# Performance work log

Hardware: AMD Instinct MI355X
Metric: run time of the kernel (lower is better)

## Reference

```python
import jax, jax.numpy as jnp
import numpy as np

N_NODES = 40000


def _sage_conv(x, edge_index, W_l, W_r, b, num_nodes):
    # PyG SAGEConv (mean aggr): out = lin_l(mean_{j in N(i)} x_j) + lin_r(x_i)
    src, dst = edge_index[0], edge_index[1]
    msgs = x[src]                                            # [E, F] gather
    sums = jax.ops.segment_sum(msgs, dst, num_segments=num_nodes)
    counts = jax.ops.segment_sum(jnp.ones((src.shape[0],), x.dtype), dst,
                                 num_segments=num_nodes)
    mean = sums / jnp.maximum(counts, 1.0)[:, None]          # [N, F]
    return mean @ W_l + b + x @ W_r


def setup_inputs() -> dict:
    key = jax.random.key(0)
    ks = jax.random.split(key, 8)
    in_c, hid_c, out_c = 128, 256, 128
    x = jax.random.normal(ks[0], (N_NODES, in_c), dtype=jnp.float32)
    edge_index = jax.random.randint(ks[1], (2, 640000), 0, N_NODES, dtype=jnp.int64)
    s1 = 1.0 / np.sqrt(in_c)
    s2 = 1.0 / np.sqrt(hid_c)
    return {
        "x": x,
        "edge_index": edge_index,
        "W1_l": jax.random.uniform(ks[2], (in_c, hid_c), jnp.float32, -s1, s1),
        "W1_r": jax.random.uniform(ks[3], (in_c, hid_c), jnp.float32, -s1, s1),
        "b1": jnp.zeros((hid_c,), jnp.float32),
        "W2_l": jax.random.uniform(ks[4], (hid_c, out_c), jnp.float32, -s2, s2),
        "W2_r": jax.random.uniform(ks[5], (hid_c, out_c), jnp.float32, -s2, s2),
        "b2": jnp.zeros((out_c,), jnp.float32),
    }


def reference(x, edge_index, W1_l, W1_r, b1, W2_l, W2_r, b2):
    h = _sage_conv(x, edge_index, W1_l, W1_r, b1, N_NODES)
    h = jax.nn.relu(h)
    out = _sage_conv(h, edge_index, W2_l, W2_r, b2, N_NODES)
    return out
```

## Files before the change

kernel.cpp:

```cpp
#include <hip/hip_runtime.h>


constexpr int F1  = 128;
constexpr int HID = 256;

typedef __attribute__((ext_vector_type(8))) short   short8;
typedef __attribute__((ext_vector_type(8))) ushort  us8;
typedef __attribute__((ext_vector_type(4))) ushort  us4;
typedef __attribute__((ext_vector_type(4))) float   f32x4;

__device__ __forceinline__ ushort f2bf(float f) {
  unsigned u = __float_as_uint(f);
  return (ushort)((u + 0x7fffu + ((u >> 16) & 1u)) >> 16);
}
__device__ __forceinline__ float bf2f_lo(unsigned v) { return __uint_as_float(v << 16); }
__device__ __forceinline__ float bf2f_hi(unsigned v) { return __uint_as_float(v & 0xffff0000u); }

#define GLOAD_LDS16(gsrc, ldst)                                                  \
  __builtin_amdgcn_global_load_lds(                                              \
      (const __attribute__((address_space(1))) void*)(gsrc),                     \
      (__attribute__((address_space(3))) void*)(ldst), 16, 0, 0)

__global__ void deg_kernel(const int* __restrict__ dst, int* __restrict__ deg, int E) {
  int i = (blockIdx.x * blockDim.x + threadIdx.x) * 2;
  if (i + 1 < E) {
    int2 d = *(const int2*)(dst + i);
    atomicAdd(deg + d.x, 1);
    atomicAdd(deg + d.y, 1);
  } else if (i < E) {
    atomicAdd(deg + dst[i], 1);
  }
}

__global__ __launch_bounds__(256) void scan_part(const int* __restrict__ deg,
                                                 int* __restrict__ bsum, int N) {
  __shared__ int sm[256];
  int t = threadIdx.x;
  int base = blockIdx.x * 1024 + t * 4;
  int s = 0;
  if (base + 3 < N) {
    int4 v = *(const int4*)(deg + base);
    s = v.x + v.y + v.z + v.w;
  } else {
    for (int q = 0; q < 4; ++q) if (base + q < N) s += deg[base + q];
  }
  sm[t] = s;
  __syncthreads();
  for (int d = 128; d; d >>= 1) {
    if (t < d) sm[t] += sm[t + d];
    __syncthreads();
  }
  if (t == 0) bsum[blockIdx.x] = sm[0];
}

__global__ void scan_bsum(const int* __restrict__ bsum, int* __restrict__ boff,
                          int* __restrict__ off, int N, int nb) {
  int t = threadIdx.x;
  int v = (t < nb) ? bsum[t] : 0;
  int inc = v;
  for (int d = 1; d < 64; d <<= 1) {
    int u = __shfl_up(inc, d);
    if (t >= d) inc += u;
  }
  if (t < nb) boff[t] = inc - v;
  if (t == 63) off[N] = inc;
}

__global__ __launch_bounds__(256) void scan_emit(const int* __restrict__ deg,
                                                 const int* __restrict__ boff,
                                                 int* __restrict__ off,
                                                 int* __restrict__ cursor, int N) {
  __shared__ int sm[256];
  int t = threadIdx.x;
  int base = blockIdx.x * 1024 + t * 4;
  int d0 = 0, d1 = 0, d2 = 0, d3 = 0;
  if (base + 3 < N) {
    int4 v = *(const int4*)(deg + base);
    d0 = v.x; d1 = v.y; d2 = v.z; d3 = v.w;
  } else {
    if (base + 0 < N) d0 = deg[base + 0];
    if (base + 1 < N) d1 = deg[base + 1];
    if (base + 2 < N) d2 = deg[base + 2];
    if (base + 3 < N) d3 = deg[base + 3];
  }
  int s = d0 + d1 + d2 + d3;
  sm[t] = s;
  __syncthreads();
  for (int d = 1; d < 256; d <<= 1) {
    int u = (t >= d) ? sm[t - d] : 0;
    __syncthreads();
    sm[t] += u;
    __syncthreads();
  }
  int o0 = (t ? sm[t - 1] : 0) + boff[blockIdx.x];
  int o1 = o0 + d0, o2 = o1 + d1, o3 = o2 + d2;
  if (base + 3 < N) {
    int4 o = make_int4(o0, o1, o2, o3);
    *(int4*)(off + base) = o;
    *(int4*)(cursor + base) = o;
  } else {
    if (base + 0 < N) { off[base + 0] = o0; cursor[base + 0] = o0; }
    if (base + 1 < N) { off[base + 1] = o1; cursor[base + 1] = o1; }
    if (base + 2 < N) { off[base + 2] = o2; cursor[base + 2] = o2; }
    if (base + 3 < N) { off[base + 3] = o3; cursor[base + 3] = o3; }
  }
}

__global__ void fill_kernel(const int* __restrict__ src, const int* __restrict__ dst,
                            int* __restrict__ cursor, int* __restrict__ csr, int E) {
  int i = blockIdx.x * blockDim.x + threadIdx.x;
  if (i < E) {
    int p = atomicAdd(cursor + dst[i], 1);
    csr[p] = src[i];
  }
}

__global__ void xcvt_kernel(const float* __restrict__ x, ushort* __restrict__ Ab,
                            int* __restrict__ deg, int N) {
  int i = blockIdx.x * blockDim.x + threadIdx.x;
  if (i < N) deg[i] = 0;
  if (i >= N * 16) return;
  int row = i >> 4, c = (i & 15) * 8;
  const float* p = x + (size_t)row * F1 + c;
  us8 o;
#pragma unroll
  for (int j = 0; j < 8; ++j) o[j] = f2bf(p[j]);
  *(us8*)(Ab + (size_t)row * HID + 128 + c) = o;
}

__global__ void wcvt_kernel(const float* __restrict__ W1l, const float* __restrict__ W1r,
                            const float* __restrict__ W2l, const float* __restrict__ W2r,
                            ushort* __restrict__ B1t, ushort* __restrict__ B2t) {
  int i = blockIdx.x * blockDim.x + threadIdx.x;
  if (i >= 16384) return;
  int which = i >> 13;
  int j = i & 8191;
  int n = j >> 5;
  int kb = (j & 31) * 8;
  us8 o;
  if (which == 0) {
#pragma unroll
    for (int q = 0; q < 8; ++q) {
      int k = kb + q;
      float v = (k < 128) ? W1l[k * HID + n] : W1r[(k - 128) * HID + n];
      o[q] = f2bf(v);
    }
    *(us8*)(B1t + n * HID + kb) = o;
  } else {
#pragma unroll
    for (int q = 0; q < 8; ++q) {
      int k = kb + q;
      float v = (n < 128) ? W2l[k * F1 + n] : W2r[k * F1 + (n - 128)];
      o[q] = f2bf(v);
    }
    *(us8*)(B2t + n * HID + kb) = o;
  }
}


__device__ __forceinline__ void acc8(float* acc, const uint4 v) {
  acc[0] += bf2f_lo(v.x); acc[1] += bf2f_hi(v.x);
  acc[2] += bf2f_lo(v.y); acc[3] += bf2f_hi(v.y);
  acc[4] += bf2f_lo(v.z); acc[5] += bf2f_hi(v.z);
  acc[6] += bf2f_lo(v.w); acc[7] += bf2f_hi(v.w);
}

__global__ __launch_bounds__(256) void agg1_kernel(const int* __restrict__ off,
                                                   const int* __restrict__ csr,
                                                   ushort* __restrict__ Ab, int N) {
  const int t = threadIdx.x;
  const int w = t >> 6, l = t & 63;
  const int g = l >> 4, sub = l & 15;
  const int node = blockIdx.x * 16 + w * 4 + g;
  if (node >= N) return;
  const int s = off[node], e = off[node + 1];
  float acc[8] = {0.f, 0.f, 0.f, 0.f, 0.f, 0.f, 0.f, 0.f};
  const int cb = sub * 8;
  const int4* csr4 = (const int4*)csr;
  int k0 = s & ~7;
  int4 c0 = csr4[(k0 >> 2) + 0];
  int4 c1 = csr4[(k0 >> 2) + 1];
#define ROW1(j) (*(const uint4*)(Ab + (size_t)(j) * HID + 128 + cb))
  for (int k = k0; k < e; k += 8) {
    int4 n0 = csr4[(k >> 2) + 2];
    int4 n1 = csr4[(k >> 2) + 3];
    if (k + 0 >= s && k + 0 < e) acc8(acc, ROW1(c0.x));
    if (k + 1 >= s && k + 1 < e) acc8(acc, ROW1(c0.y));
    if (k + 2 >= s && k + 2 < e) acc8(acc, ROW1(c0.z));
    if (k + 3 >= s && k + 3 < e) acc8(acc, ROW1(c0.w));
    if (k + 4 >= s && k + 4 < e) acc8(acc, ROW1(c1.x));
    if (k + 5 >= s && k + 5 < e) acc8(acc, ROW1(c1.y));
    if (k + 6 >= s && k + 6 < e) acc8(acc, ROW1(c1.z));
    if (k + 7 < e)               acc8(acc, ROW1(c1.w));
    c0 = n0; c1 = n1;
  }
#undef ROW1
  int d = e - s; if (d < 1) d = 1;
  float inv = 1.0f / (float)d;
  us8 o;
#pragma unroll
  for (int q = 0; q < 8; ++q) o[q] = f2bf(acc[q] * inv);
  *(us8*)(Ab + (size_t)node * HID + cb) = o;
}

__global__ __launch_bounds__(256) void agg2_kernel(const ushort* __restrict__ y2,
                                                   const int* __restrict__ off,
                                                   const int* __restrict__ csr,
                                                   float* __restrict__ out, int N) {
  const int t = threadIdx.x;
  const int w = t >> 6, l = t & 63;
  const int g = l >> 4, sub = l & 15;
  const int node = blockIdx.x * 16 + w * 4 + g;
  if (node >= N) return;
  const int s = off[node], e = off[node + 1];
  float acc[8] = {0.f, 0.f, 0.f, 0.f, 0.f, 0.f, 0.f, 0.f};
  const int cb = sub * 8;
  const int4* csr4 = (const int4*)csr;
  int k0 = s & ~7;
  int4 c0 = csr4[(k0 >> 2) + 0];
  int4 c1 = csr4[(k0 >> 2) + 1];
#define ROW2(j) (*(const uint4*)(y2 + (size_t)(j) * F1 + cb))
  for (int k = k0; k < e; k += 8) {
    int4 n0 = csr4[(k >> 2) + 2];
    int4 n1 = csr4[(k >> 2) + 3];
    if (k + 0 >= s && k + 0 < e) acc8(acc, ROW2(c0.x));
    if (k + 1 >= s && k + 1 < e) acc8(acc, ROW2(c0.y));
    if (k + 2 >= s && k + 2 < e) acc8(acc, ROW2(c0.z));
    if (k + 3 >= s && k + 3 < e) acc8(acc, ROW2(c0.w));
    if (k + 4 >= s && k + 4 < e) acc8(acc, ROW2(c1.x));
    if (k + 5 >= s && k + 5 < e) acc8(acc, ROW2(c1.y));
    if (k + 6 >= s && k + 6 < e) acc8(acc, ROW2(c1.z));
    if (k + 7 < e)               acc8(acc, ROW2(c1.w));
    c0 = n0; c1 = n1;
  }
#undef ROW2
  int d = e - s; if (d < 1) d = 1;
  float inv = 1.0f / (float)d;
  float* po = out + (size_t)node * F1 + cb;
  float4 z0 = *(const float4*)(po);
  float4 z1 = *(const float4*)(po + 4);
  z0.x += acc[0] * inv; z0.y += acc[1] * inv; z0.z += acc[2] * inv; z0.w += acc[3] * inv;
  z1.x += acc[4] * inv; z1.y += acc[5] * inv; z1.z += acc[6] * inv; z1.w += acc[7] * inv;
  *(float4*)(po)     = z0;
  *(float4*)(po + 4) = z1;
}

template <int MODE>
__global__ __launch_bounds__(256) void gemm_kernel(
    const ushort* __restrict__ A, const ushort* __restrict__ Bt,
    const float* __restrict__ bias, ushort* __restrict__ Cb,
    float* __restrict__ Cf, int M) {
  constexpr int K = 256, BK = 64;
  __shared__ __align__(16) ushort As[128 * 64];
  __shared__ __align__(16) ushort Bs[128 * 64];
  const int t = threadIdx.x;
  const int l = t & 63;
  const int w = t >> 6;
  const int m0 = blockIdx.x * 128;
  const int n0 = blockIdx.y * 128;
  const int wr = (w & 1) * 64;
  const int wc = (w >> 1) * 64;

  const int sk = (((l & 7) ^ (l >> 3)) << 3);
  const int rsub = l >> 3;

  f32x4 acc[4][4];
  const f32x4 zero = {0.f, 0.f, 0.f, 0.f};
#pragma unroll
  for (int mi = 0; mi < 4; ++mi)
#pragma unroll
    for (int ni = 0; ni < 4; ++ni) acc[mi][ni] = zero;

  for (int k0 = 0; k0 < K; k0 += BK) {
    if (k0) __syncthreads();
#pragma unroll
    for (int q = 0; q < 4; ++q) {
      int r = w * 32 + q * 8 + rsub;
      int ar = m0 + r; if (ar >= M) ar = M - 1;
      GLOAD_LDS16(A + (size_t)ar * K + k0 + sk, &As[w * 2048 + q * 512]);
      GLOAD_LDS16(Bt + (size_t)(n0 + r) * K + k0 + sk, &Bs[w * 2048 + q * 512]);
    }
    __syncthreads();
#pragma unroll
    for (int ks = 0; ks < 2; ++ks) {
      short8 af[4], bfr[4];
      const int kin = ks * 64 + ((l >> 4) << 4);
#pragma unroll
      for (int i = 0; i < 4; ++i) {
        int rA = wr + i * 16 + (l & 15);
        af[i] = *(const short8*)((const char*)As + rA * 128 + (kin ^ ((rA & 7) << 4)));
        int rB = wc + i * 16 + (l & 15);
        bfr[i] = *(const short8*)((const char*)Bs + rB * 128 + (kin ^ ((rB & 7) << 4)));
      }
#pragma unroll
      for (int mi = 0; mi < 4; ++mi)
#pragma unroll
        for (int ni = 0; ni < 4; ++ni)
          acc[mi][ni] = __builtin_amdgcn_mfma_f32_16x16x32_bf16(bfr[ni], af[mi], acc[mi][ni], 0, 0, 0);
    }
  }

#pragma unroll
  for (int ni = 0; ni < 4; ++ni) {
    const int cn = wc + ni * 16 + ((l >> 4) << 2);
    float4 bb = make_float4(0.f, 0.f, 0.f, 0.f);
    if (MODE == 1) bb = *(const float4*)(bias + n0 + cn);
    if (MODE == 2 && n0 != 0) bb = *(const float4*)(bias + cn);
#pragma unroll
    for (int mi = 0; mi < 4; ++mi) {
      int row = m0 + wr + mi * 16 + (l & 15);
      if (row >= M) continue;
      f32x4 v = acc[mi][ni];
      if (MODE == 1) {
        us4 o;
        o[0] = f2bf(fmaxf(v[0] + bb.x, 0.f));
        o[1] = f2bf(fmaxf(v[1] + bb.y, 0.f));
        o[2] = f2bf(fmaxf(v[2] + bb.z, 0.f));
        o[3] = f2bf(fmaxf(v[3] + bb.w, 0.f));
        *(us4*)(Cb + (size_t)row * HID + n0 + cn) = o;
      } else if (n0 == 0) {
        us4 o;
        o[0] = f2bf(v[0]); o[1] = f2bf(v[1]); o[2] = f2bf(v[2]); o[3] = f2bf(v[3]);
        *(us4*)(Cb + (size_t)row * F1 + cn) = o;
      } else {
        float4 o;
        o.x = v[0] + bb.x; o.y = v[1] + bb.y; o.z = v[2] + bb.z; o.w = v[3] + bb.w;
        *(float4*)(Cf + (size_t)row * F1 + cn) = o;
      }
    }
  }
}

extern "C" void kernel_launch(void* const* d_in, const int* in_sizes, int n_in,
                              void* d_out, int out_size, void* d_ws, size_t ws_size,
                              hipStream_t stream) {
  const float* x   = (const float*)d_in[0];
  const int* edge  = (const int*)d_in[1];
  const float* W1l = (const float*)d_in[2];
  const float* W1r = (const float*)d_in[3];
  const float* b1  = (const float*)d_in[4];
  const float* W2l = (const float*)d_in[5];
  const float* W2r = (const float*)d_in[6];
  const float* b2  = (const float*)d_in[7];
  float* out = (float*)d_out;

  const int N = in_sizes[0] / F1;
  const int E = in_sizes[1] / 2;
  const int* src = edge;
  const int* dst = edge + E;

  uintptr_t p = (uintptr_t)d_ws;
  auto alloc = [&](size_t bytes) -> void* {
    void* r = (void*)p;
    p += (bytes + 255) & ~(size_t)255;
    return r;
  };
  int* deg      = (int*)alloc((size_t)N * 4);
  int* off      = (int*)alloc((size_t)(N + 1) * 4);
  int* cursor   = (int*)alloc((size_t)N * 4);
  int* csr      = (int*)alloc((size_t)(E + 16) * 4);
  int* bsum     = (int*)alloc(64 * 4);
  int* boff     = (int*)alloc(64 * 4);
  ushort* Abf   = (ushort*)alloc((size_t)N * HID * 2);
  ushort* h     = (ushort*)alloc((size_t)N * HID * 2);
  ushort* y2    = (ushort*)alloc((size_t)N * F1 * 2);
  ushort* B1t   = (ushort*)alloc((size_t)HID * HID * 2);
  ushort* B2t   = (ushort*)alloc((size_t)HID * HID * 2);
  (void)ws_size; (void)n_in; (void)out_size;

  wcvt_kernel<<<64, 256, 0, stream>>>(W1l, W1r, W2l, W2r, B1t, B2t);
  xcvt_kernel<<<(N * 16 + 255) / 256, 256, 0, stream>>>(x, Abf, deg, N);
  deg_kernel<<<(E / 2 + 255) / 256, 256, 0, stream>>>(dst, deg, E);

  const int nb = (N + 1023) / 1024;
  scan_part<<<nb, 256, 0, stream>>>(deg, bsum, N);
  scan_bsum<<<1, 64, 0, stream>>>(bsum, boff, off, N, nb);
  scan_emit<<<nb, 256, 0, stream>>>(deg, boff, off, cursor, N);

  fill_kernel<<<(E + 255) / 256, 256, 0, stream>>>(src, dst, cursor, csr, E);
  agg1_kernel<<<(N + 15) / 16, 256, 0, stream>>>(off, csr, Abf, N);

  dim3 gg((N + 127) / 128, 2);
  gemm_kernel<1><<<gg, 256, 0, stream>>>(Abf, B1t, b1, h, nullptr, N);
  gemm_kernel<2><<<gg, 256, 0, stream>>>(h, B2t, b2, y2, out, N);

  agg2_kernel<<<(N + 15) / 16, 256, 0, stream>>>(y2, off, csr, out, N);
}
```

Baseline: 239.0 us.

## Fuse both GEMMs into one kernel keeping hidden activations in LDS

Merges the two GEMM launches into one mlp_kernel that computes the 64-row hidden tile, applies bias and ReLU, stores it swizzled in LDS, then runs the second GEMM from LDS. This removes the global write and read of the N×256 bf16 hidden tensor and one launch. It also merges the weight and feature conversion kernels into one and folds the block-sum scan into scan_emit. The cost is a large LDS footprint (about 72 KB per block), which lowers occupancy, and B1/B2 are reloaded by every 64-row block.

```diff
diff --git a/kernel.cpp b/kernel.cpp
--- a/kernel.cpp
+++ b/kernel.cpp
@@ -20,6 +20,48 @@
   __builtin_amdgcn_global_load_lds(                                              \
       (const __attribute__((address_space(1))) void*)(gsrc),                     \
       (__attribute__((address_space(3))) void*)(ldst), 16, 0, 0)
+
+__global__ void prep_kernel(const float* __restrict__ x, ushort* __restrict__ Ab,
+                            int* __restrict__ deg,
+                            const float* __restrict__ W1l, const float* __restrict__ W1r,
+                            const float* __restrict__ W2l, const float* __restrict__ W2r,
+                            ushort* __restrict__ B1t, ushort* __restrict__ B2t, int N) {
+  int i = blockIdx.x * blockDim.x + threadIdx.x;
+  if (i < N) deg[i] = 0;
+  if (i < N * 16) {
+    int row = i >> 4, c = (i & 15) * 8;
+    const float* p = x + (size_t)row * F1 + c;
+    us8 o;
+#pragma unroll
+    for (int j = 0; j < 8; ++j) o[j] = f2bf(p[j]);
+    *(us8*)(Ab + (size_t)row * HID + 128 + c) = o;
+    return;
+  }
+  int j = i - N * 16;
+  if (j >= 16384) return;
+  int which = j >> 13;
+  int jj = j & 8191;
+  int n = jj >> 5;
+  int kb = (jj & 31) * 8;
+  us8 o;
+  if (which == 0) {
+#pragma unroll
+    for (int q = 0; q < 8; ++q) {
+      int k = kb + q;
+      float v = (k < 128) ? W1l[k * HID + n] : W1r[(k - 128) * HID + n];
+      o[q] = f2bf(v);
+    }
+    *(us8*)(B1t + n * HID + kb) = o;
+  } else {
+#pragma unroll
+    for (int q = 0; q < 8; ++q) {
+      int k = kb + q;
+      float v = (n < 128) ? W2l[k * F1 + n] : W2r[k * F1 + (n - 128)];
+      o[q] = f2bf(v);
+    }
+    *(us8*)(B2t + n * HID + kb) = o;
+  }
+}
 
 __global__ void deg_kernel(const int* __restrict__ dst, int* __restrict__ deg, int E) {
   int i = (blockIdx.x * blockDim.x + threadIdx.x) * 2;
@@ -53,25 +95,23 @@
   if (t == 0) bsum[blockIdx.x] = sm[0];
 }
 
-__global__ void scan_bsum(const int* __restrict__ bsum, int* __restrict__ boff,
-                          int* __restrict__ off, int N, int nb) {
+__global__ __launch_bounds__(256) void scan_emit(const int* __restrict__ deg,
+                                                 const int* __restrict__ bsum,
+                                                 int* __restrict__ off,
+                                                 int* __restrict__ cursor, int N, int nb) {
+  __shared__ int sm[256];
+  __shared__ int sboff;
   int t = threadIdx.x;
-  int v = (t < nb) ? bsum[t] : 0;
-  int inc = v;
-  for (int d = 1; d < 64; d <<= 1) {
-    int u = __shfl_up(inc, d);
-    if (t >= d) inc += u;
-  }
-  if (t < nb) boff[t] = inc - v;
-  if (t == 63) off[N] = inc;
-}
-
-__global__ __launch_bounds__(256) void scan_emit(const int* __restrict__ deg,
-                                                 const int* __restrict__ boff,
-                                                 int* __restrict__ off,
-                                                 int* __restrict__ cursor, int N) {
-  __shared__ int sm[256];
-  int t = threadIdx.x;
+  if (t < 64) {
+    int v = (t < nb) ? bsum[t] : 0;
+    int inc = v;
+    for (int d = 1; d < 64; d <<= 1) {
+      int u = __shfl_up(inc, d);
+      if (t >= d) inc += u;
+    }
+    if (t == (int)blockIdx.x) sboff = inc - v;
+    if ((int)blockIdx.x == (int)gridDim.x - 1 && t == 63) off[N] = inc;
+  }
   int base = blockIdx.x * 1024 + t * 4;
   int d0 = 0, d1 = 0, d2 = 0, d3 = 0;
   if (base + 3 < N) {
@@ -92,7 +132,7 @@
     sm[t] += u;
     __syncthreads();
   }
-  int o0 = (t ? sm[t - 1] : 0) + boff[blockIdx.x];
+  int o0 = (t ? sm[t - 1] : 0) + sboff;
   int o1 = o0 + d0, o2 = o1 + d1, o3 = o2 + d2;
   if (base + 3 < N) {
     int4 o = make_int4(o0, o1, o2, o3);
@@ -114,49 +154,6 @@
     csr[p] = src[i];
   }
 }
-
-__global__ void xcvt_kernel(const float* __restrict__ x, ushort* __restrict__ Ab,
-                            int* __restrict__ deg, int N) {
-  int i = blockIdx.x * blockDim.x + threadIdx.x;
-  if (i < N) deg[i] = 0;
-  if (i >= N * 16) return;
-  int row = i >> 4, c = (i & 15) * 8;
-  const float* p = x + (size_t)row * F1 + c;
-  us8 o;
-#pragma unroll
-  for (int j = 0; j < 8; ++j) o[j] = f2bf(p[j]);
-  *(us8*)(Ab + (size_t)row * HID + 128 + c) = o;
-}
-
-__global__ void wcvt_kernel(const float* __restrict__ W1l, const float* __restrict__ W1r,
-                            const float* __restrict__ W2l, const float* __restrict__ W2r,
-                            ushort* __restrict__ B1t, ushort* __restrict__ B2t) {
-  int i = blockIdx.x * blockDim.x + threadIdx.x;
-  if (i >= 16384) return;
-  int which = i >> 13;
-  int j = i & 8191;
-  int n = j >> 5;
-  int kb = (j & 31) * 8;
-  us8 o;
-  if (which == 0) {
-#pragma unroll
-    for (int q = 0; q < 8; ++q) {
-      int k = kb + q;
-      float v = (k < 128) ? W1l[k * HID + n] : W1r[(k - 128) * HID + n];
-      o[q] = f2bf(v);
-    }
-    *(us8*)(B1t + n * HID + kb) = o;
-  } else {
-#pragma unroll
-    for (int q = 0; q < 8; ++q) {
-      int k = kb + q;
-      float v = (n < 128) ? W2l[k * F1 + n] : W2r[k * F1 + (n - 128)];
-      o[q] = f2bf(v);
-    }
-    *(us8*)(B2t + n * HID + kb) = o;
-  }
-}
-
 
 __device__ __forceinline__ void acc8(float* acc, const uint4 v) {
   acc[0] += bf2f_lo(v.x); acc[1] += bf2f_hi(v.x);
@@ -245,22 +242,22 @@
   *(float4*)(po + 4) = z1;
 }
 
-template <int MODE>
-__global__ __launch_bounds__(256) void gemm_kernel(
-    const ushort* __restrict__ A, const ushort* __restrict__ Bt,
-    const float* __restrict__ bias, ushort* __restrict__ Cb,
-    float* __restrict__ Cf, int M) {
+__global__ __launch_bounds__(256) void mlp_kernel(
+    const ushort* __restrict__ A, const ushort* __restrict__ B1t,
+    const ushort* __restrict__ B2t, const float* __restrict__ b1,
+    const float* __restrict__ b2, ushort* __restrict__ y2,
+    float* __restrict__ outp, int M) {
   constexpr int K = 256, BK = 64;
-  __shared__ __align__(16) ushort As[128 * 64];
-  __shared__ __align__(16) ushort Bs[128 * 64];
+  __shared__ __align__(16) ushort hs[64 * 256];
+  __shared__ __align__(16) ushort xreg[4096 + 16384];
+  ushort* As  = xreg;
+  ushort* B1s = xreg + 4096;
+  ushort* B2s = xreg;
   const int t = threadIdx.x;
   const int l = t & 63;
   const int w = t >> 6;
-  const int m0 = blockIdx.x * 128;
-  const int n0 = blockIdx.y * 128;
-  const int wr = (w & 1) * 64;
-  const int wc = (w >> 1) * 64;
-
+  const int m0 = blockIdx.x * 64;
+  const int wc = w * 64;
   const int sk = (((l & 7) ^ (l >> 3)) << 3);
   const int rsub = l >> 3;
 
@@ -274,11 +271,20 @@
   for (int k0 = 0; k0 < K; k0 += BK) {
     if (k0) __syncthreads();
 #pragma unroll
+    for (int q = 0; q < 2; ++q) {
+      int r = w * 16 + q * 8 + rsub;
+      int ar = m0 + r; if (ar >= M) ar = M - 1;
+      GLOAD_LDS16(A + (size_t)ar * K + k0 + sk, &As[w * 1024 + q * 512]);
+    }
+#pragma unroll
     for (int q = 0; q < 4; ++q) {
-      int r = w * 32 + q * 8 + rsub;
-      int ar = m0 + r; if (ar >= M) ar = M - 1;
-      GLOAD_LDS16(A + (size_t)ar * K + k0 + sk, &As[w * 2048 + q * 512]);
-      GLOAD_LDS16(Bt + (size_t)(n0 + r) * K + k0 + sk, &Bs[w * 2048 + q * 512]);
+      int r = w * 64 + q * 16 + (rsub + ((q & 1) ? 0 : 0)) + 0;
+      (void)r;
+    }
+#pragma unroll
+    for (int q = 0; q < 8; ++q) {
+      int r = w * 64 + q * 8 + rsub;
+      GLOAD_LDS16(B1t + (size_t)r * K + k0 + sk, &B1s[w * 4096 + q * 512]);
     }
     __syncthreads();
 #pragma unroll
@@ -287,10 +293,10 @@
       const int kin = ks * 64 + ((l >> 4) << 4);
 #pragma unroll
       for (int i = 0; i < 4; ++i) {
-        int rA = wr + i * 16 + (l & 15);
+        int rA = i * 16 + (l & 15);
         af[i] = *(const short8*)((const char*)As + rA * 128 + (kin ^ ((rA & 7) << 4)));
         int rB = wc + i * 16 + (l & 15);
-        bfr[i] = *(const short8*)((const char*)Bs + rB * 128 + (kin ^ ((rB & 7) << 4)));
+        bfr[i] = *(const short8*)((const char*)B1s + rB * 128 + (kin ^ ((rB & 7) << 4)));
       }
 #pragma unroll
       for (int mi = 0; mi < 4; ++mi)
@@ -299,33 +305,75 @@
           acc[mi][ni] = __builtin_amdgcn_mfma_f32_16x16x32_bf16(bfr[ni], af[mi], acc[mi][ni], 0, 0, 0);
     }
   }
-
 #pragma unroll
   for (int ni = 0; ni < 4; ++ni) {
     const int cn = wc + ni * 16 + ((l >> 4) << 2);
-    float4 bb = make_float4(0.f, 0.f, 0.f, 0.f);
-    if (MODE == 1) bb = *(const float4*)(bias + n0 + cn);
-    if (MODE == 2 && n0 != 0) bb = *(const float4*)(bias + cn);
+    float4 bb = *(const float4*)(b1 + cn);
 #pragma unroll
     for (int mi = 0; mi < 4; ++mi) {
-      int row = m0 + wr + mi * 16 + (l & 15);
-      if (row >= M) continue;
+      int row = mi * 16 + (l & 15);
       f32x4 v = acc[mi][ni];
-      if (MODE == 1) {
-        us4 o;
-        o[0] = f2bf(fmaxf(v[0] + bb.x, 0.f));
-        o[1] = f2bf(fmaxf(v[1] + bb.y, 0.f));
-        o[2] = f2bf(fmaxf(v[2] + bb.z, 0.f));
-        o[3] = f2bf(fmaxf(v[3] + bb.w, 0.f));
-        *(us4*)(Cb + (size_t)row * HID + n0 + cn) = o;
-      } else if (n0 == 0) {
+      unsigned p0 = (unsigned)f2bf(fmaxf(v[0] + bb.x, 0.f)) |
+                    ((unsigned)f2bf(fmaxf(v[1] + bb.y, 0.f)) << 16);
+      unsigned p1 = (unsigned)f2bf(fmaxf(v[2] + bb.z, 0.f)) |
+                    ((unsigned)f2bf(fmaxf(v[3] + bb.w, 0.f)) << 16);
+      int byte = row * 512 + ((2 * cn) ^ ((row & 7) << 4));
+      uint2 pk; pk.x = p0; pk.y = p1;
+      *(uint2*)((char*)hs + byte) = pk;
+      acc[mi][ni] = zero;
+    }
+  }
+  __syncthreads();
+
+  for (int k0 = 0; k0 < K; k0 += BK) {
+    if (k0) __syncthreads();
+#pragma unroll
+    for (int q = 0; q < 8; ++q) {
+      int r = w * 64 + q * 8 + rsub;
+      GLOAD_LDS16(B2t + (size_t)r * K + k0 + sk, &B2s[w * 4096 + q * 512]);
+    }
+    __syncthreads();
+#pragma unroll
+    for (int ks = 0; ks < 2; ++ks) {
+      short8 af[4], bfr[4];
+      const int kin = ks * 64 + ((l >> 4) << 4);
+#pragma unroll
+      for (int i = 0; i < 4; ++i) {
+        int rA = i * 16 + (l & 15);
+        af[i] = *(const short8*)((const char*)hs + rA * 512 + ((2 * k0 + kin) ^ ((rA & 7) << 4)));
+        int rB = wc + i * 16 + (l & 15);
+        bfr[i] = *(const short8*)((const char*)B2s + rB * 128 + (kin ^ ((rB & 7) << 4)));
+      }
+#pragma unroll
+      for (int mi = 0; mi < 4; ++mi)
+#pragma unroll
+        for (int ni = 0; ni < 4; ++ni)
+          acc[mi][ni] = __builtin_amdgcn_mfma_f32_16x16x32_bf16(bfr[ni], af[mi], acc[mi][ni], 0, 0, 0);
+    }
+  }
+#pragma unroll
+  for (int ni = 0; ni < 4; ++ni) {
+    const int cn = wc + ni * 16 + ((l >> 4) << 2);
+    if (wc < 128) {
+#pragma unroll
+      for (int mi = 0; mi < 4; ++mi) {
+        int row = m0 + mi * 16 + (l & 15);
+        if (row >= M) continue;
+        f32x4 v = acc[mi][ni];
         us4 o;
         o[0] = f2bf(v[0]); o[1] = f2bf(v[1]); o[2] = f2bf(v[2]); o[3] = f2bf(v[3]);
-        *(us4*)(Cb + (size_t)row * F1 + cn) = o;
-      } else {
+        *(us4*)(y2 + (size_t)row * F1 + cn) = o;
+      }
+    } else {
+      float4 bb = *(const float4*)(b2 + (cn - 128));
+#pragma unroll
+      for (int mi = 0; mi < 4; ++mi) {
+        int row = m0 + mi * 16 + (l & 15);
+        if (row >= M) continue;
+        f32x4 v = acc[mi][ni];
         float4 o;
         o.x = v[0] + bb.x; o.y = v[1] + bb.y; o.z = v[2] + bb.z; o.w = v[3] + bb.w;
-        *(float4*)(Cf + (size_t)row * F1 + cn) = o;
+        *(float4*)(outp + (size_t)row * F1 + (cn - 128)) = o;
       }
     }
   }
@@ -360,29 +408,24 @@
   int* cursor   = (int*)alloc((size_t)N * 4);
   int* csr      = (int*)alloc((size_t)(E + 16) * 4);
   int* bsum     = (int*)alloc(64 * 4);
-  int* boff     = (int*)alloc(64 * 4);
   ushort* Abf   = (ushort*)alloc((size_t)N * HID * 2);
-  ushort* h     = (ushort*)alloc((size_t)N * HID * 2);
   ushort* y2    = (ushort*)alloc((size_t)N * F1 * 2);
   ushort* B1t   = (ushort*)alloc((size_t)HID * HID * 2);
   ushort* B2t   = (ushort*)alloc((size_t)HID * HID * 2);
   (void)ws_size; (void)n_in; (void)out_size;
 
-  wcvt_kernel<<<64, 256, 0, stream>>>(W1l, W1r, W2l, W2r, B1t, B2t);
-  xcvt_kernel<<<(N * 16 + 255) / 256, 256, 0, stream>>>(x, Abf, deg, N);
+  prep_kernel<<<(N * 16 + 16384 + 255) / 256, 256, 0, stream>>>(
+      x, Abf, deg, W1l, W1r, W2l, W2r, B1t, B2t, N);
   deg_kernel<<<(E / 2 + 255) / 256, 256, 0, stream>>>(dst, deg, E);
 
   const int nb = (N + 1023) / 1024;
   scan_part<<<nb, 256, 0, stream>>>(deg, bsum, N);
-  scan_bsum<<<1, 64, 0, stream>>>(bsum, boff, off, N, nb);
-  scan_emit<<<nb, 256, 0, stream>>>(deg, boff, off, cursor, N);
+  scan_emit<<<nb, 256, 0, stream>>>(deg, bsum, off, cursor, N, nb);
 
   fill_kernel<<<(E + 255) / 256, 256, 0, stream>>>(src, dst, cursor, csr, E);
   agg1_kernel<<<(N + 15) / 16, 256, 0, stream>>>(off, csr, Abf, N);
 
-  dim3 gg((N + 127) / 128, 2);
-  gemm_kernel<1><<<gg, 256, 0, stream>>>(Abf, B1t, b1, h, nullptr, N);
-  gemm_kernel<2><<<gg, 256, 0, stream>>>(h, B2t, b2, y2, out, N);
+  mlp_kernel<<<(N + 63) / 64, 256, 0, stream>>>(Abf, B1t, B2t, b1, b2, y2, out, N);
 
   agg2_kernel<<<(N + 15) / 16, 256, 0, stream>>>(y2, off, csr, out, N);
 }
```

New measurement: 232.9 us. -2.5%, faster.
